# Performance work log

Hardware: AMD Instinct MI355X
Metric: run time of the kernel (lower is better)

## Reference

```python
import jax, jax.numpy as jnp
import numpy as np

PI = 3.141592653589793


def _nearest_idx(g, size):
    # PyTorch grid_sample nearest, align_corners=False: unnormalize then round half up
    x = ((g + 1.0) * size - 1.0) / 2.0
    return jnp.clip(jnp.floor(x + 0.5).astype(jnp.int32), 0, size - 1)


def setup_inputs() -> dict:
    key = jax.random.key(0)
    ks = jax.random.split(key, 12)
    B, Q, H, W, C, Cf = 1, 65536, 64, 64, 256, 128
    scale = 4  # HR is 256x256
    inp = {
        'inp_img': jax.random.uniform(ks[0], (B, 3, H, W), jnp.float32),
        'coef': jax.random.normal(ks[1], (B, C, H, W), jnp.float32) * 0.5,
        'freq': jax.random.normal(ks[2], (B, Cf, H, W), jnp.float32) * 0.5,
        'coord': jax.random.uniform(ks[3], (B, Q, 2), jnp.float32, minval=-1.0, maxval=1.0),
        'cell': jnp.full((B, Q, 2), 2.0 / (H * scale), jnp.float32),
        'w_coord_fc': jax.random.normal(ks[4], (128, 2), jnp.float32) * 0.5,
        'w_phase': jax.random.normal(ks[5], (128, 2), jnp.float32) * 0.5,
        'w1': jax.random.normal(ks[6], (256, 256), jnp.float32) * (1.0 / 16.0),
        'b1': jnp.zeros((256,), jnp.float32),
        'w2': jax.random.normal(ks[7], (256, 256), jnp.float32) * (1.0 / 16.0),
        'b2': jnp.zeros((256,), jnp.float32),
        'w3': jax.random.normal(ks[8], (3, 256), jnp.float32) * (1.0 / 16.0),
        'b3': jnp.zeros((3,), jnp.float32),
    }
    return inp


def reference(inp_img, coef, freq, coord, cell, w_coord_fc, w_phase, w1, b1, w2, b2, w3, b3):
    B, C, H, W = coef.shape
    Q = coord.shape[1]
    eps = 1e-6
    rx = 1.0 / H  # 2/H/2
    ry = 1.0 / W
    # 4 local-ensemble offsets in loop order (vx,vy) in {-1,1}x{-1,1}
    offs = jnp.array([[-1.0, -1.0], [-1.0, 1.0], [1.0, -1.0], [1.0, 1.0]], jnp.float32)
    shift = offs * jnp.array([rx, ry], jnp.float32) + eps  # [4,2]
    coord_ = jnp.clip(coord[:, None, :, :] + shift[None, :, None, :], -1.0 + eps, 1.0 - eps)  # [B,4,Q,2]

    # coord channel 0 -> H axis, channel 1 -> W axis (after flip(-1) in torch)
    iy = _nearest_idx(coord_[..., 0], H)  # [B,4,Q]
    ix = _nearest_idx(coord_[..., 1], W)
    lin = iy * W + ix  # [B,4,Q]

    def gather(fmap):  # fmap [B,Cc,H,W] -> [B,4,Q,Cc]
        Cc = fmap.shape[1]
        flat = fmap.reshape(B, Cc, H * W).transpose(0, 2, 1)  # [B,HW,Cc]
        return jax.vmap(lambda f, i: f[i])(flat, lin.reshape(B, -1)).reshape(B, 4, Q, Cc)

    q_coef = gather(coef)   # [B,4,Q,256]
    q_freq = gather(freq)   # [B,4,Q,128]

    # feat_coord at nearest pixel = pixel centers from make_coord
    qc_y = -1.0 + (2.0 * iy.astype(jnp.float32) + 1.0) / H
    qc_x = -1.0 + (2.0 * ix.astype(jnp.float32) + 1.0) / W
    rel0 = (coord[:, None, :, 0] - qc_y) * H  # [B,4,Q]
    rel1 = (coord[:, None, :, 1] - qc_x) * W
    rel_coord = jnp.stack([rel0, rel1], axis=-1)  # [B,4,Q,2]
    rel_cell = cell * jnp.array([H, W], jnp.float32)  # [B,Q,2]

    q_freq = q_freq * jnp.einsum('boqd,kd->boqk', rel_coord, w_coord_fc)
    q_freq = q_freq + jnp.einsum('bqd,kd->bqk', rel_cell, w_phase)[:, None]
    q_freq = jnp.concatenate([jnp.cos(PI * q_freq), jnp.sin(PI * q_freq)], axis=-1)  # [B,4,Q,256]

    x = q_coef * q_freq
    h = jax.nn.relu(jnp.einsum('boqc,dc->boqd', x, w1) + b1)
    h = jax.nn.relu(jnp.einsum('boqc,dc->boqd', h, w2) + b2)
    preds = jnp.einsum('boqc,dc->boqd', h, w3) + b3  # [B,4,Q,3]

    area = jnp.abs(rel0 * rel1) + 1e-9  # [B,4,Q]
    tot = jnp.sum(area, axis=1, keepdims=True)
    weights = area[:, ::-1] / tot  # swap 0<->3, 1<->2
    ret = jnp.sum(preds * weights[..., None], axis=1)  # [B,Q,3]

    # bilinear grid_sample of inp_img, padding_mode='border', align_corners=False
    hi, wi = inp_img.shape[-2:]
    gy = jnp.clip(((coord[..., 0] + 1.0) * hi - 1.0) / 2.0, 0.0, hi - 1.0)
    gx = jnp.clip(((coord[..., 1] + 1.0) * wi - 1.0) / 2.0, 0.0, wi - 1.0)
    y0 = jnp.floor(gy).astype(jnp.int32); x0 = jnp.floor(gx).astype(jnp.int32)
    y1 = jnp.clip(y0 + 1, 0, hi - 1); x1 = jnp.clip(x0 + 1, 0, wi - 1)
    wy = gy - y0.astype(jnp.float32); wx = gx - x0.astype(jnp.float32)
    img_flat = inp_img.reshape(B, 3, hi * wi).transpose(0, 2, 1)  # [B,HW,3]
    g = lambda yy, xx: jax.vmap(lambda f, i: f[i])(img_flat, yy * wi + xx)  # [B,Q,3]
    samp = (g(y0, x0) * ((1 - wy) * (1 - wx))[..., None]
            + g(y0, x1) * ((1 - wy) * wx)[..., None]
            + g(y1, x0) * (wy * (1 - wx))[..., None]
            + g(y1, x1) * (wy * wx)[..., None])
    return ret + samp
```

## Files before the change

### kernel.cpp

```cpp
#include <hip/hip_runtime.h>
#include <math.h>

typedef __bf16 bf16_t;
typedef bf16_t bf16x8 __attribute__((ext_vector_type(8)));
typedef bf16_t bf16x4 __attribute__((ext_vector_type(4)));
typedef float  f32x4  __attribute__((ext_vector_type(4)));

constexpr int H = 64, W = 64, Q = 65536;
constexpr int C = 256, CF = 128;
constexpr int QPB = 32;
constexpr int PADC = 264;

#define BAR() asm volatile("s_waitcnt lgkmcnt(0)\n\ts_barrier" ::: "memory")


__global__ void transpose_cvt_kernel(const float* __restrict__ src, bf16_t* __restrict__ dst, int Crows) {
    __shared__ float tile[32][33];
    int bx = blockIdx.x * 32;
    int by = blockIdx.y * 32;
    int tx = threadIdx.x & 31;
    int ty = threadIdx.x >> 5;
#pragma unroll
    for (int i = 0; i < 4; i++)
        tile[ty + i * 8][tx] = src[(by + ty + i * 8) * 4096 + bx + tx];
    __syncthreads();
#pragma unroll
    for (int i = 0; i < 4; i++)
        dst[(bx + ty + i * 8) * Crows + by + tx] = (bf16_t)tile[tx][ty + i * 8];
}

__global__ void cvt_w_kernel(const float* __restrict__ w1, const float* __restrict__ w2,
                             bf16_t* __restrict__ w1b, bf16_t* __restrict__ w2b) {
    int i = blockIdx.x * 256 + threadIdx.x;
    w1b[i] = (bf16_t)w1[i];
    w2b[i] = (bf16_t)w2[i];
}

__global__ void pack_tab_kernel(const float* __restrict__ wcf, const float* __restrict__ wph,
                                float4* __restrict__ wtab) {
    int k = threadIdx.x;
    float4 v;
    v.x = wcf[k * 2 + 0]; v.y = wcf[k * 2 + 1];
    v.z = wph[k * 2 + 0]; v.w = wph[k * 2 + 1];
    wtab[k] = v;
}

__global__ void cvt_w3_kernel(const float* __restrict__ w3, bf16_t* __restrict__ w3p) {
    int k = threadIdx.x;
#pragma unroll
    for (int n = 0; n < 16; n++)
        w3p[n * 256 + k] = (n < 3) ? (bf16_t)w3[n * 256 + k] : (bf16_t)0.f;
}


#define LOADB(dst, Wptr, kb)                                                                  \
    {                                                                                         \
        dst[0] = *(const bf16x8*)((Wptr) + (wv * 32 + l15) * 256 + (kb) * 32 + l16 * 8);      \
        dst[1] = *(const bf16x8*)((Wptr) + (wv * 32 + 16 + l15) * 256 + (kb) * 32 + l16 * 8); \
    }

__global__ __launch_bounds__(512, 4)
void lte_fused_kernel(const bf16_t* __restrict__ coefT,
                      const bf16_t* __restrict__ freqT,
                      const bf16_t* __restrict__ w1b,
                      const bf16_t* __restrict__ w2b,
                      const bf16_t* __restrict__ w3p,
                      const float4* __restrict__ wtab,
                      const float* __restrict__ img,
                      const float* __restrict__ coord,
                      const float* __restrict__ cell,
                      const float* __restrict__ b1,
                      const float* __restrict__ b2,
                      const float* __restrict__ b3,
                      float* __restrict__ out)
{
    extern __shared__ char smem[];
    bf16_t* buf    = (bf16_t*)smem;
    float*  areaS  = (float*)(smem + 67584);
    float*  predsS = (float*)(smem + 68096);

    const int t    = threadIdx.x;
    const int lane = t & 63;
    const int wv   = t >> 6;
    const int l15  = lane & 15;
    const int l16  = lane >> 4;

    {
        const int row = t >> 2;
        const int t4  = t & 3;
        const int qL  = row >> 2;
        const int o   = row & 3;
        const int q   = blockIdx.x * QPB + qL;
        const float c0  = coord[q * 2 + 0];
        const float c1  = coord[q * 2 + 1];
        const float rc0 = cell[q * 2 + 0] * (float)H;
        const float rc1 = cell[q * 2 + 1] * (float)W;
        const float vx = (o & 2) ? 1.f : -1.f;
        const float vy = (o & 1) ? 1.f : -1.f;
        const float EPS = 1e-6f;
        float g0 = fminf(fmaxf(c0 + vx * (1.f / H) + EPS, -1.f + EPS), 1.f - EPS);
        float g1 = fminf(fmaxf(c1 + vy * (1.f / W) + EPS, -1.f + EPS), 1.f - EPS);
        int iy = (int)floorf(((g0 + 1.f) * (float)H - 1.f) * 0.5f + 0.5f);
        iy = min(max(iy, 0), H - 1);
        int ix = (int)floorf(((g1 + 1.f) * (float)W - 1.f) * 0.5f + 0.5f);
        ix = min(max(ix, 0), W - 1);
        const float rel0 = (c0 - (-1.f + (2.f * (float)iy + 1.f) / (float)H)) * (float)H;
        const float rel1 = (c1 - (-1.f + (2.f * (float)ix + 1.f) / (float)W)) * (float)W;
        if (t4 == 0) areaS[row] = fabsf(rel0 * rel1) + 1e-9f;
        const int pix = iy * W + ix;
        const bf16_t* fq = freqT + pix * CF;
        const bf16_t* cf = coefT + pix * C;
        const int k0 = t4 * 32;

        bf16x8 fqv[4], ccv[4], csv[4];
#pragma unroll
        for (int i = 0; i < 4; i++) {
            fqv[i] = *(const bf16x8*)(fq + k0 + i * 8);
            ccv[i] = *(const bf16x8*)(cf + k0 + i * 8);
            csv[i] = *(const bf16x8*)(cf + 128 + k0 + i * 8);
        }
#pragma unroll
        for (int i = 0; i < 4; i++) {
            bf16x8 vc, vs;
#pragma unroll
            for (int j = 0; j < 8; j++) {
                const int k = k0 + i * 8 + j;
                const float4 tv = wtab[k];
                const float proj = rel0 * tv.x + rel1 * tv.y;
                const float ph   = rc0 * tv.z + rc1 * tv.w;
                const float m = (float)fqv[i][j] * proj + ph;
                const float xr  = __builtin_amdgcn_fractf(m * 0.5f);
                const float s   = __builtin_amdgcn_sinf(xr);
                const float cst = __builtin_amdgcn_cosf(xr);
                vc[j] = (bf16_t)((float)ccv[i][j] * cst);
                vs[j] = (bf16_t)((float)csv[i][j] * s);
            }
            *(bf16x8*)(buf + row * PADC + k0 + i * 8)       = vc;
            *(bf16x8*)(buf + row * PADC + 128 + k0 + i * 8) = vs;
        }
    }

    bf16x8 b1q[8][2];
    LOADB(b1q[0], w1b, 0);
    LOADB(b1q[1], w1b, 1);
    BAR();

    bf16x8 b2q[8][2];
    {
        f32x4 acc[8][2];
#pragma unroll
        for (int mi = 0; mi < 8; mi++)
#pragma unroll
            for (int nf = 0; nf < 2; nf++) {
                f32x4 z = {0.f, 0.f, 0.f, 0.f};
                acc[mi][nf] = z;
            }
#pragma unroll
        for (int kb = 0; kb < 8; kb++) {
            if (kb < 6) { LOADB(b1q[kb + 2], w1b, kb + 2); }
            bf16x8 a[8];
#pragma unroll
            for (int mi = 0; mi < 8; mi++)
                a[mi] = *(bf16x8*)(buf + (mi * 16 + l15) * PADC + kb * 32 + l16 * 8);
#pragma unroll
            for (int mi = 0; mi < 8; mi++)
#pragma unroll
                for (int nf = 0; nf < 2; nf++)
                    acc[mi][nf] = __builtin_amdgcn_mfma_f32_16x16x32_bf16(b1q[kb][nf], a[mi], acc[mi][nf], 0, 0, 0);
        }
        LOADB(b2q[0], w2b, 0);
        LOADB(b2q[1], w2b, 1);
        BAR();
#pragma unroll
        for (int nf = 0; nf < 2; nf++) {
            const int colb = wv * 32 + nf * 16 + l16 * 4;
            const float4 bv = *(const float4*)(b1 + colb);
#pragma unroll
            for (int mi = 0; mi < 8; mi++) {
                const int row = mi * 16 + l15;
                bf16x4 h;
                h[0] = (bf16_t)fmaxf(acc[mi][nf][0] + bv.x, 0.f);
                h[1] = (bf16_t)fmaxf(acc[mi][nf][1] + bv.y, 0.f);
                h[2] = (bf16_t)fmaxf(acc[mi][nf][2] + bv.z, 0.f);
                h[3] = (bf16_t)fmaxf(acc[mi][nf][3] + bv.w, 0.f);
                *(bf16x4*)(buf + row * PADC + colb) = h;
            }
        }
        BAR();
    }

    {
        f32x4 acc[8][2];
#pragma unroll
        for (int mi = 0; mi < 8; mi++)
#pragma unroll
            for (int nf = 0; nf < 2; nf++) {
                f32x4 z = {0.f, 0.f, 0.f, 0.f};
                acc[mi][nf] = z;
            }
#pragma unroll
        for (int kb = 0; kb < 8; kb++) {
            if (kb < 6) { LOADB(b2q[kb + 2], w2b, kb + 2); }
            bf16x8 a[8];
#pragma unroll
            for (int mi = 0; mi < 8; mi++)
                a[mi] = *(bf16x8*)(buf + (mi * 16 + l15) * PADC + kb * 32 + l16 * 8);
#pragma unroll
            for (int mi = 0; mi < 8; mi++)
#pragma unroll
                for (int nf = 0; nf < 2; nf++)
                    acc[mi][nf] = __builtin_amdgcn_mfma_f32_16x16x32_bf16(b2q[kb][nf], a[mi], acc[mi][nf], 0, 0, 0);
        }
        BAR();
#pragma unroll
        for (int nf = 0; nf < 2; nf++) {
            const int colb = wv * 32 + nf * 16 + l16 * 4;
            const float4 bv = *(const float4*)(b2 + colb);
#pragma unroll
            for (int mi = 0; mi < 8; mi++) {
                const int row = mi * 16 + l15;
                bf16x4 h;
                h[0] = (bf16_t)fmaxf(acc[mi][nf][0] + bv.x, 0.f);
                h[1] = (bf16_t)fmaxf(acc[mi][nf][1] + bv.y, 0.f);
                h[2] = (bf16_t)fmaxf(acc[mi][nf][2] + bv.z, 0.f);
                h[3] = (bf16_t)fmaxf(acc[mi][nf][3] + bv.w, 0.f);
                *(bf16x4*)(buf + row * PADC + colb) = h;
            }
        }
        BAR();
    }

    {
        f32x4 acc3 = {0.f, 0.f, 0.f, 0.f};
#pragma unroll
        for (int kb = 0; kb < 8; kb++) {
            bf16x8 a = *(bf16x8*)(buf + (wv * 16 + l15) * PADC + kb * 32 + l16 * 8);
            bf16x8 b = *(const bf16x8*)(w3p + l15 * 256 + kb * 32 + l16 * 8);
            acc3 = __builtin_amdgcn_mfma_f32_16x16x32_bf16(a, b, acc3, 0, 0, 0);
        }
        if (l15 < 3) {
            const float bv = b3[l15];
#pragma unroll
            for (int r = 0; r < 4; r++) {
                const int row = wv * 16 + l16 * 4 + r;
                predsS[row * 3 + l15] = acc3[r] + bv;
            }
        }
    }
    BAR();

    if (t < QPB) {
        const int qL = t;
        const int q  = blockIdx.x * QPB + qL;
        const int r0 = qL * 4;
        const float a0 = areaS[r0 + 0], a1 = areaS[r0 + 1], a2 = areaS[r0 + 2], a3 = areaS[r0 + 3];
        const float inv = 1.f / (a0 + a1 + a2 + a3);
        const float wgt0 = a3 * inv, wgt1 = a2 * inv, wgt2 = a1 * inv, wgt3 = a0 * inv;
        const float c0 = coord[q * 2 + 0];
        const float c1 = coord[q * 2 + 1];
        float gy = fminf(fmaxf(((c0 + 1.f) * (float)H - 1.f) * 0.5f, 0.f), (float)(H - 1));
        float gx = fminf(fmaxf(((c1 + 1.f) * (float)W - 1.f) * 0.5f, 0.f), (float)(W - 1));
        int y0 = (int)floorf(gy); int x0 = (int)floorf(gx);
        int y1 = min(y0 + 1, H - 1); int x1 = min(x0 + 1, W - 1);
        const float wy = gy - (float)y0, wx = gx - (float)x0;
#pragma unroll
        for (int ch = 0; ch < 3; ch++) {
            const float ret = predsS[(r0 + 0) * 3 + ch] * wgt0 + predsS[(r0 + 1) * 3 + ch] * wgt1
                            + predsS[(r0 + 2) * 3 + ch] * wgt2 + predsS[(r0 + 3) * 3 + ch] * wgt3;
            const float* ip = img + ch * 4096;
            const float v00 = ip[y0 * 64 + x0], v01 = ip[y0 * 64 + x1];
            const float v10 = ip[y1 * 64 + x0], v11 = ip[y1 * 64 + x1];
            const float samp = v00 * (1.f - wy) * (1.f - wx) + v01 * (1.f - wy) * wx
                             + v10 * wy * (1.f - wx) + v11 * wy * wx;
            out[q * 3 + ch] = ret + samp;
        }
    }
}


extern "C" void kernel_launch(void* const* d_in, const int* in_sizes, int n_in,
                              void* d_out, int out_size, void* d_ws, size_t ws_size,
                              hipStream_t stream) {
    const float* img   = (const float*)d_in[0];
    const float* coef  = (const float*)d_in[1];
    const float* freq  = (const float*)d_in[2];
    const float* coord = (const float*)d_in[3];
    const float* cell  = (const float*)d_in[4];
    const float* wcf   = (const float*)d_in[5];
    const float* wph   = (const float*)d_in[6];
    const float* w1    = (const float*)d_in[7];
    const float* b1    = (const float*)d_in[8];
    const float* w2    = (const float*)d_in[9];
    const float* b2    = (const float*)d_in[10];
    const float* w3    = (const float*)d_in[11];
    const float* b3    = (const float*)d_in[12];
    float* out = (float*)d_out;

    char* ws = (char*)d_ws;
    bf16_t* coefT = (bf16_t*)ws;
    bf16_t* freqT = (bf16_t*)(ws + 2097152);
    bf16_t* w1b   = (bf16_t*)(ws + 3145728);
    bf16_t* w2b   = (bf16_t*)(ws + 3276800);
    float4* wtab  = (float4*)(ws + 3407872);
    bf16_t* w3p   = (bf16_t*)(ws + 3409920);

    transpose_cvt_kernel<<<dim3(128, 8), 256, 0, stream>>>(coef, coefT, 256);
    transpose_cvt_kernel<<<dim3(128, 4), 256, 0, stream>>>(freq, freqT, 128);
    cvt_w_kernel<<<256, 256, 0, stream>>>(w1, w2, w1b, w2b);
    pack_tab_kernel<<<1, 128, 0, stream>>>(wcf, wph, wtab);
    cvt_w3_kernel<<<1, 256, 0, stream>>>(w3, w3p);

    const size_t ldsBytes = 69632;
    lte_fused_kernel<<<Q / QPB, 512, ldsBytes, stream>>>(
        coefT, freqT, w1b, w2b, w3p, wtab, img, coord, cell, b1, b2, b3, out);
}
```

Before: 167.2 us.

## Split block into two half-tiles and overlap gather/sincos with MLP MFMA

Each block's 128 rows are split into two 64-row halves held in separate LDS buffers. The second half's feature gather and sin/cos encoding are interleaved with the first half's layer-1 MFMA, and layer 3 plus the final combine of half A are overlapped with half B's layers. MFMA loops raise wave priority with s_setprio, and the combine step is spread over 48 threads, one per query-channel pair. This aims to hide global gather latency and transcendental ALU work behind matrix math, at the cost of more barriers, smaller MFMA tiles per pass, and weights reloaded for each half.

```diff
diff --git a/kernel.cpp b/kernel.cpp
--- a/kernel.cpp
+++ b/kernel.cpp
@@ -57,6 +57,152 @@
     {                                                                                         \
         dst[0] = *(const bf16x8*)((Wptr) + (wv * 32 + l15) * 256 + (kb) * 32 + l16 * 8);      \
         dst[1] = *(const bf16x8*)((Wptr) + (wv * 32 + 16 + l15) * 256 + (kb) * 32 + l16 * 8); \
+    }
+
+__device__ __forceinline__ void stage_gather(
+    const bf16_t* __restrict__ coefT, const bf16_t* __restrict__ freqT,
+    const float* __restrict__ coord, const float* __restrict__ cell,
+    int q, int o, int k0,
+    bf16x8* fqv, bf16x8* ccv, bf16x8* csv,
+    float& rel0, float& rel1, float& rc0, float& rc1, float& area)
+{
+    const float c0 = coord[q * 2 + 0];
+    const float c1 = coord[q * 2 + 1];
+    rc0 = cell[q * 2 + 0] * (float)H;
+    rc1 = cell[q * 2 + 1] * (float)W;
+    const float vx = (o & 2) ? 1.f : -1.f;
+    const float vy = (o & 1) ? 1.f : -1.f;
+    const float EPS = 1e-6f;
+    float g0 = fminf(fmaxf(c0 + vx * (1.f / H) + EPS, -1.f + EPS), 1.f - EPS);
+    float g1 = fminf(fmaxf(c1 + vy * (1.f / W) + EPS, -1.f + EPS), 1.f - EPS);
+    int iy = (int)floorf(((g0 + 1.f) * (float)H - 1.f) * 0.5f + 0.5f);
+    iy = min(max(iy, 0), H - 1);
+    int ix = (int)floorf(((g1 + 1.f) * (float)W - 1.f) * 0.5f + 0.5f);
+    ix = min(max(ix, 0), W - 1);
+    rel0 = (c0 - (-1.f + (2.f * (float)iy + 1.f) / (float)H)) * (float)H;
+    rel1 = (c1 - (-1.f + (2.f * (float)ix + 1.f) / (float)W)) * (float)W;
+    area = fabsf(rel0 * rel1) + 1e-9f;
+    const int pix = iy * W + ix;
+    const bf16_t* fq = freqT + pix * CF;
+    const bf16_t* cf = coefT + pix * C;
+#pragma unroll
+    for (int i = 0; i < 2; i++) {
+        fqv[i] = *(const bf16x8*)(fq + k0 + i * 8);
+        ccv[i] = *(const bf16x8*)(cf + k0 + i * 8);
+        csv[i] = *(const bf16x8*)(cf + 128 + k0 + i * 8);
+    }
+}
+
+__device__ __forceinline__ void stage_finish(
+    const float4* __restrict__ wtab, bf16_t* buf, int row, int k0,
+    const bf16x8* fqv, const bf16x8* ccv, const bf16x8* csv,
+    float rel0, float rel1, float rc0, float rc1)
+{
+#pragma unroll
+    for (int i = 0; i < 2; i++) {
+        bf16x8 vc, vs;
+#pragma unroll
+        for (int j = 0; j < 8; j++) {
+            const int k = k0 + i * 8 + j;
+            const float4 tv = wtab[k];
+            const float m = (float)fqv[i][j] * (rel0 * tv.x + rel1 * tv.y) + (rc0 * tv.z + rc1 * tv.w);
+            const float xr = __builtin_amdgcn_fractf(m * 0.5f);
+            vc[j] = (bf16_t)((float)ccv[i][j] * __builtin_amdgcn_cosf(xr));
+            vs[j] = (bf16_t)((float)csv[i][j] * __builtin_amdgcn_sinf(xr));
+        }
+        *(bf16x8*)(buf + row * PADC + k0 + i * 8)       = vc;
+        *(bf16x8*)(buf + row * PADC + 128 + k0 + i * 8) = vs;
+    }
+}
+
+#define LAYER64(BUF, QUEUE, WPTR, ACC)                                                        \
+    {                                                                                         \
+        __builtin_amdgcn_s_setprio(1);                                                        \
+        _Pragma("unroll")                                                                     \
+        for (int kb = 0; kb < 8; kb++) {                                                      \
+            if (kb < 6) { LOADB(QUEUE[kb + 2], WPTR, kb + 2); }                               \
+            bf16x8 a[4];                                                                      \
+            _Pragma("unroll")                                                                 \
+            for (int mi = 0; mi < 4; mi++)                                                    \
+                a[mi] = *(bf16x8*)((BUF) + (mi * 16 + l15) * PADC + kb * 32 + l16 * 8);       \
+            _Pragma("unroll")                                                                 \
+            for (int mi = 0; mi < 4; mi++)                                                    \
+                _Pragma("unroll")                                                             \
+                for (int nf = 0; nf < 2; nf++)                                                \
+                    ACC[mi][nf] = __builtin_amdgcn_mfma_f32_16x16x32_bf16(QUEUE[kb][nf], a[mi], ACC[mi][nf], 0, 0, 0); \
+        }                                                                                     \
+        __builtin_amdgcn_s_setprio(0);                                                        \
+    }
+
+#define ZEROACC(ACC)                                                                          \
+    _Pragma("unroll")                                                                         \
+    for (int mi = 0; mi < 4; mi++)                                                            \
+        _Pragma("unroll")                                                                     \
+        for (int nf = 0; nf < 2; nf++) {                                                      \
+            f32x4 z = {0.f, 0.f, 0.f, 0.f};                                                   \
+            ACC[mi][nf] = z;                                                                  \
+        }
+
+#define WRITEBACK64(BUF, BIAS, ACC)                                                           \
+    _Pragma("unroll")                                                                         \
+    for (int nf = 0; nf < 2; nf++) {                                                          \
+        const int colb = wv * 32 + nf * 16 + l16 * 4;                                         \
+        const float4 bv = *(const float4*)((BIAS) + colb);                                    \
+        _Pragma("unroll")                                                                     \
+        for (int mi = 0; mi < 4; mi++) {                                                      \
+            const int row_ = mi * 16 + l15;                                                   \
+            bf16x4 hh;                                                                        \
+            hh[0] = (bf16_t)fmaxf(ACC[mi][nf][0] + bv.x, 0.f);                                \
+            hh[1] = (bf16_t)fmaxf(ACC[mi][nf][1] + bv.y, 0.f);                                \
+            hh[2] = (bf16_t)fmaxf(ACC[mi][nf][2] + bv.z, 0.f);                                \
+            hh[3] = (bf16_t)fmaxf(ACC[mi][nf][3] + bv.w, 0.f);                                \
+            *(bf16x4*)((BUF) + row_ * PADC + colb) = hh;                                      \
+        }                                                                                     \
+    }
+
+#define L3TILE(BUF, PBASE)                                                                    \
+    if (wv < 4) {                                                                             \
+        f32x4 acc3 = {0.f, 0.f, 0.f, 0.f};                                                    \
+        _Pragma("unroll")                                                                     \
+        for (int kb = 0; kb < 8; kb++) {                                                      \
+            bf16x8 a = *(bf16x8*)((BUF) + (wv * 16 + l15) * PADC + kb * 32 + l16 * 8);        \
+            bf16x8 b = *(const bf16x8*)(w3p + l15 * 256 + kb * 32 + l16 * 8);                 \
+            acc3 = __builtin_amdgcn_mfma_f32_16x16x32_bf16(a, b, acc3, 0, 0, 0);              \
+        }                                                                                     \
+        if (l15 < 3) {                                                                        \
+            const float bv = b3[l15];                                                         \
+            _Pragma("unroll")                                                                 \
+            for (int r = 0; r < 4; r++)                                                       \
+                predsS[((PBASE) + wv * 16 + l16 * 4 + r) * 3 + l15] = acc3[r] + bv;           \
+        }                                                                                     \
+    }
+
+#define COMBINE(QBASE, RBASE)                                                                 \
+    if (t < 48) {                                                                             \
+        const int ch = t >> 4;                                                                \
+        const int qL = t & 15;                                                                \
+        const int q_ = (QBASE) + qL;                                                          \
+        const int r0 = (RBASE) + qL * 4;                                                      \
+        const float a0 = areaS[r0 + 0], a1 = areaS[r0 + 1];                                   \
+        const float a2 = areaS[r0 + 2], a3 = areaS[r0 + 3];                                   \
+        const float inv = 1.f / (a0 + a1 + a2 + a3);                                          \
+        const float ret = predsS[(r0 + 0) * 3 + ch] * a3 * inv                                \
+                        + predsS[(r0 + 1) * 3 + ch] * a2 * inv                                \
+                        + predsS[(r0 + 2) * 3 + ch] * a1 * inv                                \
+                        + predsS[(r0 + 3) * 3 + ch] * a0 * inv;                               \
+        const float c0 = coord[q_ * 2 + 0];                                                   \
+        const float c1 = coord[q_ * 2 + 1];                                                   \
+        float gy = fminf(fmaxf(((c0 + 1.f) * (float)H - 1.f) * 0.5f, 0.f), (float)(H - 1));   \
+        float gx = fminf(fmaxf(((c1 + 1.f) * (float)W - 1.f) * 0.5f, 0.f), (float)(W - 1));   \
+        int y0 = (int)floorf(gy); int x0 = (int)floorf(gx);                                   \
+        int y1 = min(y0 + 1, H - 1); int x1 = min(x0 + 1, W - 1);                             \
+        const float wy = gy - (float)y0, wx = gx - (float)x0;                                 \
+        const float* ip = img + ch * 4096;                                                    \
+        const float samp = ip[y0 * 64 + x0] * (1.f - wy) * (1.f - wx)                         \
+                         + ip[y0 * 64 + x1] * (1.f - wy) * wx                                 \
+                         + ip[y1 * 64 + x0] * wy * (1.f - wx)                                 \
+                         + ip[y1 * 64 + x1] * wy * wx;                                        \
+        out[q_ * 3 + ch] = ret + samp;                                                        \
     }
 
 __global__ __launch_bounds__(512, 4)
@@ -75,7 +221,8 @@
                       float* __restrict__ out)
 {
     extern __shared__ char smem[];
-    bf16_t* buf    = (bf16_t*)smem;
+    bf16_t* bufA   = (bf16_t*)smem;
+    bf16_t* bufB   = (bf16_t*)(smem + 33792);
     float*  areaS  = (float*)(smem + 67584);
     float*  predsS = (float*)(smem + 68096);
 
@@ -84,197 +231,70 @@
     const int wv   = t >> 6;
     const int l15  = lane & 15;
     const int l16  = lane >> 4;
+    const int row  = t >> 3;
+    const int t8   = t & 7;
+    const int k0   = t8 * 16;
+    const int o    = row & 3;
+    const int qrow = row >> 2;
+
+    const int qA = blockIdx.x * QPB;
+    const int qB = qA + 16;
+
+    bf16x8 bq1[8][2], bq2[8][2];
+    LOADB(bq1[0], w1b, 0);
+    LOADB(bq1[1], w1b, 1);
 
     {
-        const int row = t >> 2;
-        const int t4  = t & 3;
-        const int qL  = row >> 2;
-        const int o   = row & 3;
-        const int q   = blockIdx.x * QPB + qL;
-        const float c0  = coord[q * 2 + 0];
-        const float c1  = coord[q * 2 + 1];
-        const float rc0 = cell[q * 2 + 0] * (float)H;
-        const float rc1 = cell[q * 2 + 1] * (float)W;
-        const float vx = (o & 2) ? 1.f : -1.f;
-        const float vy = (o & 1) ? 1.f : -1.f;
-        const float EPS = 1e-6f;
-        float g0 = fminf(fmaxf(c0 + vx * (1.f / H) + EPS, -1.f + EPS), 1.f - EPS);
-        float g1 = fminf(fmaxf(c1 + vy * (1.f / W) + EPS, -1.f + EPS), 1.f - EPS);
-        int iy = (int)floorf(((g0 + 1.f) * (float)H - 1.f) * 0.5f + 0.5f);
-        iy = min(max(iy, 0), H - 1);
-        int ix = (int)floorf(((g1 + 1.f) * (float)W - 1.f) * 0.5f + 0.5f);
-        ix = min(max(ix, 0), W - 1);
-        const float rel0 = (c0 - (-1.f + (2.f * (float)iy + 1.f) / (float)H)) * (float)H;
-        const float rel1 = (c1 - (-1.f + (2.f * (float)ix + 1.f) / (float)W)) * (float)W;
-        if (t4 == 0) areaS[row] = fabsf(rel0 * rel1) + 1e-9f;
-        const int pix = iy * W + ix;
-        const bf16_t* fq = freqT + pix * CF;
-        const bf16_t* cf = coefT + pix * C;
-        const int k0 = t4 * 32;
-
-        bf16x8 fqv[4], ccv[4], csv[4];
-#pragma unroll
-        for (int i = 0; i < 4; i++) {
-            fqv[i] = *(const bf16x8*)(fq + k0 + i * 8);
-            ccv[i] = *(const bf16x8*)(cf + k0 + i * 8);
-            csv[i] = *(const bf16x8*)(cf + 128 + k0 + i * 8);
-        }
-#pragma unroll
-        for (int i = 0; i < 4; i++) {
-            bf16x8 vc, vs;
-#pragma unroll
-            for (int j = 0; j < 8; j++) {
-                const int k = k0 + i * 8 + j;
-                const float4 tv = wtab[k];
-                const float proj = rel0 * tv.x + rel1 * tv.y;
-                const float ph   = rc0 * tv.z + rc1 * tv.w;
-                const float m = (float)fqv[i][j] * proj + ph;
-                const float xr  = __builtin_amdgcn_fractf(m * 0.5f);
-                const float s   = __builtin_amdgcn_sinf(xr);
-                const float cst = __builtin_amdgcn_cosf(xr);
-                vc[j] = (bf16_t)((float)ccv[i][j] * cst);
-                vs[j] = (bf16_t)((float)csv[i][j] * s);
-            }
-            *(bf16x8*)(buf + row * PADC + k0 + i * 8)       = vc;
-            *(bf16x8*)(buf + row * PADC + 128 + k0 + i * 8) = vs;
-        }
-    }
-
-    bf16x8 b1q[8][2];
-    LOADB(b1q[0], w1b, 0);
-    LOADB(b1q[1], w1b, 1);
-    BAR();
-
-    bf16x8 b2q[8][2];
-    {
-        f32x4 acc[8][2];
-#pragma unroll
-        for (int mi = 0; mi < 8; mi++)
-#pragma unroll
-            for (int nf = 0; nf < 2; nf++) {
-                f32x4 z = {0.f, 0.f, 0.f, 0.f};
-                acc[mi][nf] = z;
-            }
-#pragma unroll
-        for (int kb = 0; kb < 8; kb++) {
-            if (kb < 6) { LOADB(b1q[kb + 2], w1b, kb + 2); }
-            bf16x8 a[8];
-#pragma unroll
-            for (int mi = 0; mi < 8; mi++)
-                a[mi] = *(bf16x8*)(buf + (mi * 16 + l15) * PADC + kb * 32 + l16 * 8);
-#pragma unroll
-            for (int mi = 0; mi < 8; mi++)
-#pragma unroll
-                for (int nf = 0; nf < 2; nf++)
-                    acc[mi][nf] = __builtin_amdgcn_mfma_f32_16x16x32_bf16(b1q[kb][nf], a[mi], acc[mi][nf], 0, 0, 0);
-        }
-        LOADB(b2q[0], w2b, 0);
-        LOADB(b2q[1], w2b, 1);
-        BAR();
-#pragma unroll
-        for (int nf = 0; nf < 2; nf++) {
-            const int colb = wv * 32 + nf * 16 + l16 * 4;
-            const float4 bv = *(const float4*)(b1 + colb);
-#pragma unroll
-            for (int mi = 0; mi < 8; mi++) {
-                const int row = mi * 16 + l15;
-                bf16x4 h;
-                h[0] = (bf16_t)fmaxf(acc[mi][nf][0] + bv.x, 0.f);
-                h[1] = (bf16_t)fmaxf(acc[mi][nf][1] + bv.y, 0.f);
-                h[2] = (bf16_t)fmaxf(acc[mi][nf][2] + bv.z, 0.f);
-                h[3] = (bf16_t)fmaxf(acc[mi][nf][3] + bv.w, 0.f);
-                *(bf16x4*)(buf + row * PADC + colb) = h;
-            }
-        }
-        BAR();
-    }
-
-    {
-        f32x4 acc[8][2];
-#pragma unroll
-        for (int mi = 0; mi < 8; mi++)
-#pragma unroll
-            for (int nf = 0; nf < 2; nf++) {
-                f32x4 z = {0.f, 0.f, 0.f, 0.f};
-                acc[mi][nf] = z;
-            }
-#pragma unroll
-        for (int kb = 0; kb < 8; kb++) {
-            if (kb < 6) { LOADB(b2q[kb + 2], w2b, kb + 2); }
-            bf16x8 a[8];
-#pragma unroll
-            for (int mi = 0; mi < 8; mi++)
-                a[mi] = *(bf16x8*)(buf + (mi * 16 + l15) * PADC + kb * 32 + l16 * 8);
-#pragma unroll
-            for (int mi = 0; mi < 8; mi++)
-#pragma unroll
-                for (int nf = 0; nf < 2; nf++)
-                    acc[mi][nf] = __builtin_amdgcn_mfma_f32_16x16x32_bf16(b2q[kb][nf], a[mi], acc[mi][nf], 0, 0, 0);
-        }
-        BAR();
-#pragma unroll
-        for (int nf = 0; nf < 2; nf++) {
-            const int colb = wv * 32 + nf * 16 + l16 * 4;
-            const float4 bv = *(const float4*)(b2 + colb);
-#pragma unroll
-            for (int mi = 0; mi < 8; mi++) {
-                const int row = mi * 16 + l15;
-                bf16x4 h;
-                h[0] = (bf16_t)fmaxf(acc[mi][nf][0] + bv.x, 0.f);
-                h[1] = (bf16_t)fmaxf(acc[mi][nf][1] + bv.y, 0.f);
-                h[2] = (bf16_t)fmaxf(acc[mi][nf][2] + bv.z, 0.f);
-                h[3] = (bf16_t)fmaxf(acc[mi][nf][3] + bv.w, 0.f);
-                *(bf16x4*)(buf + row * PADC + colb) = h;
-            }
-        }
-        BAR();
-    }
-
-    {
-        f32x4 acc3 = {0.f, 0.f, 0.f, 0.f};
-#pragma unroll
-        for (int kb = 0; kb < 8; kb++) {
-            bf16x8 a = *(bf16x8*)(buf + (wv * 16 + l15) * PADC + kb * 32 + l16 * 8);
-            bf16x8 b = *(const bf16x8*)(w3p + l15 * 256 + kb * 32 + l16 * 8);
-            acc3 = __builtin_amdgcn_mfma_f32_16x16x32_bf16(a, b, acc3, 0, 0, 0);
-        }
-        if (l15 < 3) {
-            const float bv = b3[l15];
-#pragma unroll
-            for (int r = 0; r < 4; r++) {
-                const int row = wv * 16 + l16 * 4 + r;
-                predsS[row * 3 + l15] = acc3[r] + bv;
-            }
-        }
-    }
-    BAR();
-
-    if (t < QPB) {
-        const int qL = t;
-        const int q  = blockIdx.x * QPB + qL;
-        const int r0 = qL * 4;
-        const float a0 = areaS[r0 + 0], a1 = areaS[r0 + 1], a2 = areaS[r0 + 2], a3 = areaS[r0 + 3];
-        const float inv = 1.f / (a0 + a1 + a2 + a3);
-        const float wgt0 = a3 * inv, wgt1 = a2 * inv, wgt2 = a1 * inv, wgt3 = a0 * inv;
-        const float c0 = coord[q * 2 + 0];
-        const float c1 = coord[q * 2 + 1];
-        float gy = fminf(fmaxf(((c0 + 1.f) * (float)H - 1.f) * 0.5f, 0.f), (float)(H - 1));
-        float gx = fminf(fmaxf(((c1 + 1.f) * (float)W - 1.f) * 0.5f, 0.f), (float)(W - 1));
-        int y0 = (int)floorf(gy); int x0 = (int)floorf(gx);
-        int y1 = min(y0 + 1, H - 1); int x1 = min(x0 + 1, W - 1);
-        const float wy = gy - (float)y0, wx = gx - (float)x0;
-#pragma unroll
-        for (int ch = 0; ch < 3; ch++) {
-            const float ret = predsS[(r0 + 0) * 3 + ch] * wgt0 + predsS[(r0 + 1) * 3 + ch] * wgt1
-                            + predsS[(r0 + 2) * 3 + ch] * wgt2 + predsS[(r0 + 3) * 3 + ch] * wgt3;
-            const float* ip = img + ch * 4096;
-            const float v00 = ip[y0 * 64 + x0], v01 = ip[y0 * 64 + x1];
-            const float v10 = ip[y1 * 64 + x0], v11 = ip[y1 * 64 + x1];
-            const float samp = v00 * (1.f - wy) * (1.f - wx) + v01 * (1.f - wy) * wx
-                             + v10 * wy * (1.f - wx) + v11 * wy * wx;
-            out[q * 3 + ch] = ret + samp;
-        }
-    }
+        bf16x8 fqv[2], ccv[2], csv[2];
+        float rel0, rel1, rc0, rc1, area;
+        stage_gather(coefT, freqT, coord, cell, qA + qrow, o, k0, fqv, ccv, csv, rel0, rel1, rc0, rc1, area);
+        if (t8 == 0) areaS[row] = area;
+        stage_finish(wtab, bufA, row, k0, fqv, ccv, csv, rel0, rel1, rc0, rc1);
+    }
+    BAR();
+
+    bf16x8 fqB[2], ccB[2], csB[2];
+    float rel0B, rel1B, rc0B, rc1B, areaB;
+    stage_gather(coefT, freqT, coord, cell, qB + qrow, o, k0, fqB, ccB, csB, rel0B, rel1B, rc0B, rc1B, areaB);
+    if (t8 == 0) areaS[64 + row] = areaB;
+
+    f32x4 acc[4][2];
+    ZEROACC(acc);
+    LAYER64(bufA, bq1, w1b, acc);
+    LOADB(bq2[0], w2b, 0);
+    LOADB(bq2[1], w2b, 1);
+    stage_finish(wtab, bufB, row, k0, fqB, ccB, csB, rel0B, rel1B, rc0B, rc1B);
+    BAR();
+    WRITEBACK64(bufA, b1, acc);
+    BAR();
+
+    ZEROACC(acc);
+    LAYER64(bufA, bq2, w2b, acc);
+    LOADB(bq1[0], w1b, 0);
+    LOADB(bq1[1], w1b, 1);
+    BAR();
+    WRITEBACK64(bufA, b2, acc);
+    BAR();
+
+    L3TILE(bufA, 0);
+    ZEROACC(acc);
+    LAYER64(bufB, bq1, w1b, acc);
+    LOADB(bq2[0], w2b, 0);
+    LOADB(bq2[1], w2b, 1);
+    BAR();
+    WRITEBACK64(bufB, b1, acc);
+    COMBINE(qA, 0);
+    BAR();
+
+    ZEROACC(acc);
+    LAYER64(bufB, bq2, w2b, acc);
+    BAR();
+    WRITEBACK64(bufB, b2, acc);
+    BAR();
+
+    L3TILE(bufB, 64);
+    BAR();
+    COMBINE(qB, 64);
 }
 
 
```

Result: slower. 212.6 us (+27.1%).
